# Kernel tuning notes

Measured on AMD Instinct MI355X. Metric: run time of the kernel, lower is better.

Reference implementation:

```python
import jax, jax.numpy as jnp
import numpy as np

TAU = 0.5


def _l2norm(x):
    # F.normalize(p=2, dim=1): x / max(||x||, eps) with eps=1e-12
    n = jnp.sqrt(jnp.sum(x * x, axis=1, keepdims=True))
    return x / jnp.maximum(n, 1e-12)


def setup_inputs() -> dict:
    key = jax.random.key(0)
    k1, k2 = jax.random.split(key)
    N, D = 8192, 512
    left = jax.random.normal(k1, (N, D), dtype=jnp.float32)
    right = jax.random.normal(k2, (N, D), dtype=jnp.float32)
    return {"left": left, "right": right}


def reference(left, right) -> jnp.ndarray:
    zl = _l2norm(left)
    zr = _l2norm(right)
    # [N, N] cosine-similarity matrices
    refl_sim = jnp.exp(jnp.matmul(zl, zl.T) / TAU)
    between_sim = jnp.exp(jnp.matmul(zl, zr.T) / TAU)
    between_diag = jnp.diagonal(between_sim)
    refl_diag = jnp.diagonal(refl_sim)
    denom = refl_sim.sum(axis=1) + between_sim.sum(axis=1) - refl_diag
    loss = -jnp.log(between_diag / denom)  # [N]
    return loss
```

## Files before the change

kernel.cpp:

```cpp
#include <hip/hip_runtime.h>

#define NROWS 8192
#define DDIM 512
#define ZROWS 16384
#define BM 256
#define BN 256
#define BK 64
#define KTILES (DDIM / BK)
#define NLR_BLOCKS 1024
#define NSYM_BLOCKS 528
#define NBLOCKS (NLR_BLOCKS + NSYM_BLOCKS)

typedef __attribute__((ext_vector_type(8))) short short8;
typedef __attribute__((ext_vector_type(4))) float f32x4;

__device__ __forceinline__ unsigned short f2bf(float f) {
  unsigned int u = __float_as_uint(f);
  u = (u + 0x7FFFu + ((u >> 16) & 1u)) >> 16;
  return (unsigned short)u;
}

__global__ __launch_bounds__(256) void nrm_kernel(const float* __restrict__ left,
                                                  const float* __restrict__ right,
                                                  unsigned short* __restrict__ Z,
                                                  float* __restrict__ dlr) {
  const int i = blockIdx.x;
  const int t = threadIdx.x;
  const float2 lv = ((const float2*)(left + (size_t)i * DDIM))[t];
  const float2 rv = ((const float2*)(right + (size_t)i * DDIM))[t];
  float ssl = lv.x * lv.x + lv.y * lv.y;
  float ssr = rv.x * rv.x + rv.y * rv.y;
  float slr = lv.x * rv.x + lv.y * rv.y;
#pragma unroll
  for (int m = 1; m < 64; m <<= 1) {
    ssl += __shfl_xor(ssl, m);
    ssr += __shfl_xor(ssr, m);
    slr += __shfl_xor(slr, m);
  }
  __shared__ float red[3][4];
  const int w = t >> 6;
  if ((t & 63) == 0) { red[0][w] = ssl; red[1][w] = ssr; red[2][w] = slr; }
  __syncthreads();
  ssl = red[0][0] + red[0][1] + red[0][2] + red[0][3];
  ssr = red[1][0] + red[1][1] + red[1][2] + red[1][3];
  slr = red[2][0] + red[2][1] + red[2][2] + red[2][3];
  const float invl = 1.0f / fmaxf(sqrtf(ssl), 1e-12f);
  const float invr = 1.0f / fmaxf(sqrtf(ssr), 1e-12f);
  if (t == 0) dlr[i] = slr * invl * invr;
  ushort2 zl2; zl2.x = f2bf(lv.x * invl); zl2.y = f2bf(lv.y * invl);
  ushort2 zr2; zr2.x = f2bf(rv.x * invr); zr2.y = f2bf(rv.y * invr);
  ((ushort2*)(Z + (size_t)i * DDIM))[t] = zl2;
  ((ushort2*)(Z + (size_t)(NROWS + i) * DDIM))[t] = zr2;
}

__global__ __launch_bounds__(512) void sim_kernel(const unsigned short* __restrict__ Z,
                                                  float* __restrict__ partial) {
  __shared__ __align__(16) unsigned short sA[2][BM * BK];
  __shared__ __align__(16) unsigned short sB[2][BN * BK];

  int tm, tn; bool sym = false;
  {
    const int bid = blockIdx.x;
    if (bid < NLR_BLOCKS) {
      tm = bid >> 5; tn = 32 + (bid & 31);
    } else {
      const int b2 = bid - NLR_BLOCKS;
      int i = (int)(32.5f - sqrtf(32.5f * 32.5f - 2.0f * (float)b2));
      if (i < 0) i = 0; if (i > 31) i = 31;
      while (i > 0 && (32 * i - i * (i - 1) / 2) > b2) --i;
      while (i < 31 && (32 * (i + 1) - (i + 1) * i / 2) <= b2) ++i;
      tm = i; tn = i + (b2 - (32 * i - i * (i - 1) / 2));
      sym = (tn != tm);
    }
  }

  const int t = threadIdx.x;
  const int l = t & 63;
  const int w = t >> 6;
  const int wm = w >> 2;
  const int wn = w & 3;
  const int lr = l & 15;
  const int lk = l >> 4;

  f32x4 acc[8][4];
#pragma unroll
  for (int a = 0; a < 8; ++a)
#pragma unroll
    for (int b = 0; b < 4; ++b)
#pragma unroll
      for (int r = 0; r < 4; ++r) acc[a][b][r] = 0.0f;

  const unsigned short* Abase = Z + (size_t)tm * BM * DDIM;
  const unsigned short* Bbase = Z + (size_t)tn * BN * DDIM;

  const int srow = t >> 3;
  const int scol = ((t & 7) ^ (srow & 7)) * 8;

#define STAGE_AJ(bufi, k0, j)                                                     \
  __builtin_amdgcn_global_load_lds(                                               \
      (const __attribute__((address_space(1))) void*)(Abase +                     \
          (size_t)((j) * 64 + srow) * DDIM + (k0) + scol),                        \
      (__attribute__((address_space(3))) void*)(&sA[bufi][((j) * 512 + t) * 8]),  \
      16, 0, 0);
#define STAGE_BJ(bufi, k0, j)                                                     \
  __builtin_amdgcn_global_load_lds(                                               \
      (const __attribute__((address_space(1))) void*)(Bbase +                     \
          (size_t)((j) * 64 + srow) * DDIM + (k0) + scol),                        \
      (__attribute__((address_space(3))) void*)(&sB[bufi][((j) * 512 + t) * 8]),  \
      16, 0, 0);
#define STAGE_A02(b, k0) { STAGE_AJ(b, k0, 0) STAGE_AJ(b, k0, 2) }
#define STAGE_A13(b, k0) { STAGE_AJ(b, k0, 1) STAGE_AJ(b, k0, 3) }
#define STAGE_B01(b, k0) { STAGE_BJ(b, k0, 0) STAGE_BJ(b, k0, 1) }
#define STAGE_B23(b, k0) { STAGE_BJ(b, k0, 2) STAGE_BJ(b, k0, 3) }

  short8 af[4][2], ag[4][2], bf[4][2];

#define DS_A(dst, bufi, fmb)                                                       \
  _Pragma("unroll")                                                                \
  for (int fm = 0; fm < 4; ++fm)                                                   \
    _Pragma("unroll")                                                              \
    for (int ks = 0; ks < 2; ++ks) {                                               \
      const int row = wm * 128 + ((fmb) + fm) * 16 + lr;                           \
      dst[fm][ks] = *(const short8*)&sA[bufi][row * BK + ((ks * 4 + lk) ^ (lr & 7)) * 8]; \
    }

#define DS_B2(bufi, fnb)                                                           \
  _Pragma("unroll")                                                                \
  for (int fn = 0; fn < 2; ++fn)                                                   \
    _Pragma("unroll")                                                              \
    for (int ks = 0; ks < 2; ++ks) {                                               \
      const int row = wn * 64 + ((fnb) + fn) * 16 + lr;                            \
      bf[(fnb) + fn][ks] = *(const short8*)&sB[bufi][row * BK + ((ks * 4 + lk) ^ (lr & 7)) * 8]; \
    }

#define MFMA16(A, fmb, fnb)                                                        \
  __builtin_amdgcn_s_setprio(1);                                                   \
  _Pragma("unroll")                                                                \
  for (int fm = 0; fm < 4; ++fm)                                                   \
    _Pragma("unroll")                                                              \
    for (int fn = 0; fn < 2; ++fn)                                                 \
      _Pragma("unroll")                                                            \
      for (int ks = 0; ks < 2; ++ks)                                               \
        acc[(fmb) + fm][(fnb) + fn] =                                              \
            __builtin_amdgcn_mfma_f32_16x16x32_bf16(A[fm][ks], bf[(fnb) + fn][ks], \
                                                    acc[(fmb) + fm][(fnb) + fn],   \
                                                    0, 0, 0);                      \
  __builtin_amdgcn_s_setprio(0);

#define BAR   __builtin_amdgcn_s_barrier()
#define VM6   asm volatile("s_waitcnt vmcnt(6)" ::: "memory")
#define VM0   asm volatile("s_waitcnt vmcnt(0)" ::: "memory")

  STAGE_A02(0, 0); STAGE_A13(0, 0); STAGE_B01(0, 0); STAGE_B23(0, 0);
  STAGE_A02(1, BK); STAGE_B01(1, BK); STAGE_B23(1, BK);
  VM6;
  BAR;

#pragma unroll
  for (int it = 0; it < 4; ++it) {
    const int kt = 2 * it;
    DS_A(af, 0, 0); DS_B2(0, 0);
    STAGE_A13(1, (kt + 1) * BK);
    BAR;
    MFMA16(af, 0, 0);
    BAR;
    DS_B2(0, 2);
    if (kt + 2 < KTILES) STAGE_A02(0, (kt + 2) * BK);
    BAR;
    MFMA16(af, 0, 2);
    BAR;
    DS_A(ag, 0, 4);
    if (kt + 2 < KTILES) STAGE_B01(0, (kt + 2) * BK);
    BAR;
    MFMA16(ag, 4, 0);
    BAR;
    if (kt + 2 < KTILES) { STAGE_B23(0, (kt + 2) * BK); VM6; } else { VM0; }
    BAR;
    MFMA16(ag, 4, 2);
    BAR;
    DS_A(af, 1, 0); DS_B2(1, 0);
    if (kt + 2 < KTILES) STAGE_A13(0, (kt + 2) * BK);
    BAR;
    MFMA16(af, 0, 0);
    BAR;
    DS_B2(1, 2);
    if (kt + 3 < KTILES) STAGE_A02(1, (kt + 3) * BK);
    BAR;
    MFMA16(af, 0, 2);
    BAR;
    DS_A(ag, 1, 4);
    if (kt + 3 < KTILES) STAGE_B01(1, (kt + 3) * BK);
    BAR;
    MFMA16(ag, 4, 0);
    BAR;
    if (kt + 3 < KTILES) { STAGE_B23(1, (kt + 3) * BK); VM6; } else { VM0; }
    BAR;
    MFMA16(ag, 4, 2);
    BAR;
  }

  float* rsum = (float*)&sA[0][0];
  float* csum = rsum + BM;
  if (t < BM) { rsum[t] = 0.0f; csum[t] = 0.0f; }
  __syncthreads();
  float c0 = 0.0f, c1 = 0.0f, c2 = 0.0f, c3 = 0.0f;
#pragma unroll
  for (int fm = 0; fm < 8; ++fm) {
#pragma unroll
    for (int r = 0; r < 4; ++r) {
      float e0 = __expf(2.0f * acc[fm][0][r]);
      float e1 = __expf(2.0f * acc[fm][1][r]);
      float e2 = __expf(2.0f * acc[fm][2][r]);
      float e3 = __expf(2.0f * acc[fm][3][r]);
      float v = e0 + e1 + e2 + e3;
      v += __shfl_xor(v, 1);
      v += __shfl_xor(v, 2);
      v += __shfl_xor(v, 4);
      v += __shfl_xor(v, 8);
      if (lr == 0) atomicAdd(&rsum[wm * 128 + fm * 16 + lk * 4 + r], v);
      c0 += e0; c1 += e1; c2 += e2; c3 += e3;
    }
  }
  if (sym) {
    c0 += __shfl_xor(c0, 16); c0 += __shfl_xor(c0, 32);
    c1 += __shfl_xor(c1, 16); c1 += __shfl_xor(c1, 32);
    c2 += __shfl_xor(c2, 16); c2 += __shfl_xor(c2, 32);
    c3 += __shfl_xor(c3, 16); c3 += __shfl_xor(c3, 32);
    if (l < 16) {
      atomicAdd(&csum[wn * 64 +  0 + lr], c0);
      atomicAdd(&csum[wn * 64 + 16 + lr], c1);
      atomicAdd(&csum[wn * 64 + 32 + lr], c2);
      atomicAdd(&csum[wn * 64 + 48 + lr], c3);
    }
  }
  __syncthreads();
  if (t < BM) partial[(size_t)tn * NROWS + tm * BM + t] = rsum[t];
  if (sym && t < BM) partial[(size_t)tm * NROWS + tn * BM + t] = csum[t];
}

__global__ __launch_bounds__(256) void fin_kernel(const float* __restrict__ partial,
                                                  const float* __restrict__ dlr,
                                                  float* __restrict__ out) {
  const int i = blockIdx.x * 256 + threadIdx.x;
  float s = 0.0f;
#pragma unroll 8
  for (int p = 0; p < 64; ++p) s += partial[(size_t)p * NROWS + i];
  out[i] = logf(s - 7.38905609893065f) - 2.0f * dlr[i];
}

extern "C" void kernel_launch(void* const* d_in, const int* in_sizes, int n_in,
                              void* d_out, int out_size, void* d_ws, size_t ws_size,
                              hipStream_t stream) {
  const float* left = (const float*)d_in[0];
  const float* right = (const float*)d_in[1];
  float* out = (float*)d_out;

  unsigned short* Z = (unsigned short*)d_ws;
  char* p = (char*)d_ws + (size_t)ZROWS * DDIM * 2;
  float* dlr = (float*)p;
  float* partial = (float*)(p + (size_t)NROWS * 4);

  nrm_kernel<<<NROWS, 256, 0, stream>>>(left, right, Z, dlr);
  sim_kernel<<<NBLOCKS, 512, 0, stream>>>(Z, partial);
  fin_kernel<<<NROWS / 256, 256, 0, stream>>>(partial, dlr, out);
}
```

Before: 161.6 us.

## Make sim kernel persistent and prefetch next tile during current tile's mainloop

Replaces the one-block-per-tile launch with a persistent grid of 256 blocks that loop over tiles with a fixed stride. The last k-tile stages of each tile prefetch the first k-slices of the next tile, so global loads overlap the epilogue and per-block startup cost is removed. rsum/csum move to dedicated shared arrays so the epilogue no longer overwrites the staging buffers holding the prefetched data. Risks: 1552 tiles over 256 blocks leaves a ragged tail (about 6 waves), the k-loop is no longer unrolled, and LDS use grows slightly.

```diff
diff --git a/kernel.cpp b/kernel.cpp
--- a/kernel.cpp
+++ b/kernel.cpp
@@ -6,10 +6,10 @@
 #define BM 256
 #define BN 256
 #define BK 64
-#define KTILES (DDIM / BK)
-#define NLR_BLOCKS 1024
-#define NSYM_BLOCKS 528
-#define NBLOCKS (NLR_BLOCKS + NSYM_BLOCKS)
+#define KTILES 8
+#define NLR_TILES 1024
+#define NTILES 1552
+#define GRID 256
 
 typedef __attribute__((ext_vector_type(8))) short short8;
 typedef __attribute__((ext_vector_type(4))) float f32x4;
@@ -18,6 +18,20 @@
   unsigned int u = __float_as_uint(f);
   u = (u + 0x7FFFu + ((u >> 16) & 1u)) >> 16;
   return (unsigned short)u;
+}
+
+__device__ __forceinline__ void decode_tile(int tile, int& tm, int& tn, bool& sym) {
+  if (tile < NLR_TILES) {
+    tm = tile >> 5; tn = 32 + (tile & 31); sym = false;
+  } else {
+    const int b2 = tile - NLR_TILES;
+    int i = (int)(32.5f - sqrtf(32.5f * 32.5f - 2.0f * (float)b2));
+    if (i < 0) i = 0; if (i > 31) i = 31;
+    while (i > 0 && (32 * i - i * (i - 1) / 2) > b2) --i;
+    while (i < 31 && (32 * (i + 1) - (i + 1) * i / 2) <= b2) ++i;
+    tm = i; tn = i + (b2 - (32 * i - i * (i - 1) / 2));
+    sym = (tn != tm);
+  }
 }
 
 __global__ __launch_bounds__(256) void nrm_kernel(const float* __restrict__ left,
@@ -57,22 +71,8 @@
                                                   float* __restrict__ partial) {
   __shared__ __align__(16) unsigned short sA[2][BM * BK];
   __shared__ __align__(16) unsigned short sB[2][BN * BK];
-
-  int tm, tn; bool sym = false;
-  {
-    const int bid = blockIdx.x;
-    if (bid < NLR_BLOCKS) {
-      tm = bid >> 5; tn = 32 + (bid & 31);
-    } else {
-      const int b2 = bid - NLR_BLOCKS;
-      int i = (int)(32.5f - sqrtf(32.5f * 32.5f - 2.0f * (float)b2));
-      if (i < 0) i = 0; if (i > 31) i = 31;
-      while (i > 0 && (32 * i - i * (i - 1) / 2) > b2) --i;
-      while (i < 31 && (32 * (i + 1) - (i + 1) * i / 2) <= b2) ++i;
-      tm = i; tn = i + (b2 - (32 * i - i * (i - 1) / 2));
-      sym = (tn != tm);
-    }
-  }
+  __shared__ float rsum[BM];
+  __shared__ float csum[BM];
 
   const int t = threadIdx.x;
   const int l = t & 63;
@@ -81,39 +81,31 @@
   const int wn = w & 3;
   const int lr = l & 15;
   const int lk = l >> 4;
-
-  f32x4 acc[8][4];
-#pragma unroll
-  for (int a = 0; a < 8; ++a)
-#pragma unroll
-    for (int b = 0; b < 4; ++b)
-#pragma unroll
-      for (int r = 0; r < 4; ++r) acc[a][b][r] = 0.0f;
-
+  const int srow = t >> 3;
+  const int scol = ((t & 7) ^ (srow & 7)) * 8;
+
+  int tile = blockIdx.x;
+  int tm, tn; bool sym;
+  decode_tile(tile, tm, tn, sym);
   const unsigned short* Abase = Z + (size_t)tm * BM * DDIM;
   const unsigned short* Bbase = Z + (size_t)tn * BN * DDIM;
 
-  const int srow = t >> 3;
-  const int scol = ((t & 7) ^ (srow & 7)) * 8;
-
-#define STAGE_AJ(bufi, k0, j)                                                     \
+#define GLDA(bufi, gbase, k0, j)                                                  \
   __builtin_amdgcn_global_load_lds(                                               \
-      (const __attribute__((address_space(1))) void*)(Abase +                     \
+      (const __attribute__((address_space(1))) void*)((gbase) +                   \
           (size_t)((j) * 64 + srow) * DDIM + (k0) + scol),                        \
       (__attribute__((address_space(3))) void*)(&sA[bufi][((j) * 512 + t) * 8]),  \
       16, 0, 0);
-#define STAGE_BJ(bufi, k0, j)                                                     \
+#define GLDB(bufi, gbase, k0, j)                                                  \
   __builtin_amdgcn_global_load_lds(                                               \
-      (const __attribute__((address_space(1))) void*)(Bbase +                     \
+      (const __attribute__((address_space(1))) void*)((gbase) +                   \
           (size_t)((j) * 64 + srow) * DDIM + (k0) + scol),                        \
       (__attribute__((address_space(3))) void*)(&sB[bufi][((j) * 512 + t) * 8]),  \
       16, 0, 0);
-#define STAGE_A02(b, k0) { STAGE_AJ(b, k0, 0) STAGE_AJ(b, k0, 2) }
-#define STAGE_A13(b, k0) { STAGE_AJ(b, k0, 1) STAGE_AJ(b, k0, 3) }
-#define STAGE_B01(b, k0) { STAGE_BJ(b, k0, 0) STAGE_BJ(b, k0, 1) }
-#define STAGE_B23(b, k0) { STAGE_BJ(b, k0, 2) STAGE_BJ(b, k0, 3) }
-
-  short8 af[4][2], ag[4][2], bf[4][2];
+#define STAGE_A02g(b, g, k) { GLDA(b, g, k, 0) GLDA(b, g, k, 2) }
+#define STAGE_A13g(b, g, k) { GLDA(b, g, k, 1) GLDA(b, g, k, 3) }
+#define STAGE_B01g(b, g, k) { GLDB(b, g, k, 0) GLDB(b, g, k, 1) }
+#define STAGE_B23g(b, g, k) { GLDB(b, g, k, 2) GLDB(b, g, k, 3) }
 
 #define DS_A(dst, bufi, fmb)                                                       \
   _Pragma("unroll")                                                                \
@@ -150,92 +142,108 @@
 #define BAR   __builtin_amdgcn_s_barrier()
 #define VM6   asm volatile("s_waitcnt vmcnt(6)" ::: "memory")
 #define VM0   asm volatile("s_waitcnt vmcnt(0)" ::: "memory")
-
-  STAGE_A02(0, 0); STAGE_A13(0, 0); STAGE_B01(0, 0); STAGE_B23(0, 0);
-  STAGE_A02(1, BK); STAGE_B01(1, BK); STAGE_B23(1, BK);
+#define LGKM0_BAR { asm volatile("s_waitcnt lgkmcnt(0)" ::: "memory"); BAR; }
+
+  STAGE_A02g(0, Abase, 0); STAGE_A13g(0, Abase, 0);
+  STAGE_B01g(0, Bbase, 0); STAGE_B23g(0, Bbase, 0);
+  STAGE_A02g(1, Abase, BK); STAGE_B01g(1, Bbase, BK); STAGE_B23g(1, Bbase, BK);
   VM6;
   BAR;
 
-#pragma unroll
-  for (int it = 0; it < 4; ++it) {
-    const int kt = 2 * it;
-    DS_A(af, 0, 0); DS_B2(0, 0);
-    STAGE_A13(1, (kt + 1) * BK);
-    BAR;
-    MFMA16(af, 0, 0);
-    BAR;
-    DS_B2(0, 2);
-    if (kt + 2 < KTILES) STAGE_A02(0, (kt + 2) * BK);
-    BAR;
-    MFMA16(af, 0, 2);
-    BAR;
-    DS_A(ag, 0, 4);
-    if (kt + 2 < KTILES) STAGE_B01(0, (kt + 2) * BK);
-    BAR;
-    MFMA16(ag, 4, 0);
-    BAR;
-    if (kt + 2 < KTILES) { STAGE_B23(0, (kt + 2) * BK); VM6; } else { VM0; }
-    BAR;
-    MFMA16(ag, 4, 2);
-    BAR;
-    DS_A(af, 1, 0); DS_B2(1, 0);
-    if (kt + 2 < KTILES) STAGE_A13(0, (kt + 2) * BK);
-    BAR;
-    MFMA16(af, 0, 0);
-    BAR;
-    DS_B2(1, 2);
-    if (kt + 3 < KTILES) STAGE_A02(1, (kt + 3) * BK);
-    BAR;
-    MFMA16(af, 0, 2);
-    BAR;
-    DS_A(ag, 1, 4);
-    if (kt + 3 < KTILES) STAGE_B01(1, (kt + 3) * BK);
-    BAR;
-    MFMA16(ag, 4, 0);
-    BAR;
-    if (kt + 3 < KTILES) { STAGE_B23(1, (kt + 3) * BK); VM6; } else { VM0; }
-    BAR;
-    MFMA16(ag, 4, 2);
-    BAR;
+  while (true) {
+    const int tileN = tile + GRID;
+    const bool has_next = (tileN < NTILES);
+    int tmN = tm, tnN = tn; bool symN = false;
+    if (has_next) decode_tile(tileN, tmN, tnN, symN);
+    const unsigned short* AbaseN = Z + (size_t)tmN * BM * DDIM;
+    const unsigned short* BbaseN = Z + (size_t)tnN * BN * DDIM;
+
+    f32x4 acc[8][4];
+#pragma unroll
+    for (int a = 0; a < 8; ++a)
+#pragma unroll
+      for (int b = 0; b < 4; ++b)
+#pragma unroll
+        for (int r = 0; r < 4; ++r) acc[a][b][r] = 0.0f;
+
+    short8 af[4][2], ag[4][2], bf[4][2];
+
+#pragma unroll 1
+    for (int it = 0; it < 4; ++it) {
+      const int k2 = 2 * it + 2, k3 = 2 * it + 3;
+      const bool st2 = (k2 < KTILES) || has_next;
+      const bool st3 = (k3 < KTILES) || has_next;
+      const unsigned short* A2 = (k2 < KTILES) ? Abase : AbaseN;
+      const unsigned short* B2 = (k2 < KTILES) ? Bbase : BbaseN;
+      const unsigned short* A3 = (k3 < KTILES) ? Abase : AbaseN;
+      const unsigned short* B3 = (k3 < KTILES) ? Bbase : BbaseN;
+      const int k2o = (k2 & 7) * BK;
+      const int k3o = (k3 & 7) * BK;
+      const int k1o = (2 * it + 1) * BK;
+
+      DS_A(af, 0, 0); DS_B2(0, 0);
+      STAGE_A13g(1, Abase, k1o);
+      BAR; MFMA16(af, 0, 0); BAR;
+      DS_B2(0, 2);
+      if (st2) STAGE_A02g(0, A2, k2o);
+      BAR; MFMA16(af, 0, 2); BAR;
+      DS_A(ag, 0, 4);
+      if (st2) STAGE_B01g(0, B2, k2o);
+      BAR; MFMA16(ag, 4, 0); BAR;
+      if (st2) { STAGE_B23g(0, B2, k2o); VM6; } else { VM0; }
+      BAR; MFMA16(ag, 4, 2); BAR;
+      DS_A(af, 1, 0); DS_B2(1, 0);
+      if (st2) STAGE_A13g(0, A2, k2o);
+      BAR; MFMA16(af, 0, 0); BAR;
+      DS_B2(1, 2);
+      if (st3) STAGE_A02g(1, A3, k3o);
+      BAR; MFMA16(af, 0, 2); BAR;
+      DS_A(ag, 1, 4);
+      if (st3) STAGE_B01g(1, B3, k3o);
+      BAR; MFMA16(ag, 4, 0); BAR;
+      if (st3) { STAGE_B23g(1, B3, k3o); VM6; } else { VM0; }
+      BAR; MFMA16(ag, 4, 2); BAR;
+    }
+
+    if (t < BM) { rsum[t] = 0.0f; csum[t] = 0.0f; }
+    LGKM0_BAR;
+    float c0 = 0.0f, c1 = 0.0f, c2 = 0.0f, c3 = 0.0f;
+#pragma unroll
+    for (int fm = 0; fm < 8; ++fm) {
+#pragma unroll
+      for (int r = 0; r < 4; ++r) {
+        float e0 = __expf(2.0f * acc[fm][0][r]);
+        float e1 = __expf(2.0f * acc[fm][1][r]);
+        float e2 = __expf(2.0f * acc[fm][2][r]);
+        float e3 = __expf(2.0f * acc[fm][3][r]);
+        float v = e0 + e1 + e2 + e3;
+        v += __shfl_xor(v, 1);
+        v += __shfl_xor(v, 2);
+        v += __shfl_xor(v, 4);
+        v += __shfl_xor(v, 8);
+        if (lr == 0) atomicAdd(&rsum[wm * 128 + fm * 16 + lk * 4 + r], v);
+        c0 += e0; c1 += e1; c2 += e2; c3 += e3;
+      }
+    }
+    if (sym) {
+      c0 += __shfl_xor(c0, 16); c0 += __shfl_xor(c0, 32);
+      c1 += __shfl_xor(c1, 16); c1 += __shfl_xor(c1, 32);
+      c2 += __shfl_xor(c2, 16); c2 += __shfl_xor(c2, 32);
+      c3 += __shfl_xor(c3, 16); c3 += __shfl_xor(c3, 32);
+      if (l < 16) {
+        atomicAdd(&csum[wn * 64 +  0 + lr], c0);
+        atomicAdd(&csum[wn * 64 + 16 + lr], c1);
+        atomicAdd(&csum[wn * 64 + 32 + lr], c2);
+        atomicAdd(&csum[wn * 64 + 48 + lr], c3);
+      }
+    }
+    LGKM0_BAR;
+    if (t < BM) partial[(size_t)tn * NROWS + tm * BM + t] = rsum[t];
+    if (sym && t < BM) partial[(size_t)tm * NROWS + tn * BM + t] = csum[t];
+
+    if (!has_next) break;
+    tile = tileN; tm = tmN; tn = tnN; sym = symN; Abase = AbaseN; Bbase = BbaseN;
   }
-
-  float* rsum = (float*)&sA[0][0];
-  float* csum = rsum + BM;
-  if (t < BM) { rsum[t] = 0.0f; csum[t] = 0.0f; }
-  __syncthreads();
-  float c0 = 0.0f, c1 = 0.0f, c2 = 0.0f, c3 = 0.0f;
-#pragma unroll
-  for (int fm = 0; fm < 8; ++fm) {
-#pragma unroll
-    for (int r = 0; r < 4; ++r) {
-      float e0 = __expf(2.0f * acc[fm][0][r]);
-      float e1 = __expf(2.0f * acc[fm][1][r]);
-      float e2 = __expf(2.0f * acc[fm][2][r]);
-      float e3 = __expf(2.0f * acc[fm][3][r]);
-      float v = e0 + e1 + e2 + e3;
-      v += __shfl_xor(v, 1);
-      v += __shfl_xor(v, 2);
-      v += __shfl_xor(v, 4);
-      v += __shfl_xor(v, 8);
-      if (lr == 0) atomicAdd(&rsum[wm * 128 + fm * 16 + lk * 4 + r], v);
-      c0 += e0; c1 += e1; c2 += e2; c3 += e3;
-    }
-  }
-  if (sym) {
-    c0 += __shfl_xor(c0, 16); c0 += __shfl_xor(c0, 32);
-    c1 += __shfl_xor(c1, 16); c1 += __shfl_xor(c1, 32);
-    c2 += __shfl_xor(c2, 16); c2 += __shfl_xor(c2, 32);
-    c3 += __shfl_xor(c3, 16); c3 += __shfl_xor(c3, 32);
-    if (l < 16) {
-      atomicAdd(&csum[wn * 64 +  0 + lr], c0);
-      atomicAdd(&csum[wn * 64 + 16 + lr], c1);
-      atomicAdd(&csum[wn * 64 + 32 + lr], c2);
-      atomicAdd(&csum[wn * 64 + 48 + lr], c3);
-    }
-  }
-  __syncthreads();
-  if (t < BM) partial[(size_t)tn * NROWS + tm * BM + t] = rsum[t];
-  if (sym && t < BM) partial[(size_t)tm * NROWS + tn * BM + t] = csum[t];
 }
 
 __global__ __launch_bounds__(256) void fin_kernel(const float* __restrict__ partial,
@@ -261,6 +269,6 @@
   float* partial = (float*)(p + (size_t)NROWS * 4);
 
   nrm_kernel<<<NROWS, 256, 0, stream>>>(left, right, Z, dlr);
-  sim_kernel<<<NBLOCKS, 512, 0, stream>>>(Z, partial);
+  sim_kernel<<<GRID, 512, 0, stream>>>(Z, partial);
   fin_kernel<<<NROWS / 256, 256, 0, stream>>>(partial, dlr, out);
 }
```

Result: faster. 157.4 us (-2.6%).
